# Kernel optimization log

Hardware: AMD Instinct MI355X
Metric: run time of the kernel (lower is better)

Reference implementation:

```python
import jax, jax.numpy as jnp
import numpy as np

B, L, D = 4, 512, 768
NUM_SPANS = 4096
MAX_WIDTH = 8
DFF = 4 * D


def setup_inputs() -> dict:
    key = jax.random.key(0)
    k_h, k_s, k_w, k1, k2 = jax.random.split(key, 5)
    h = jax.random.normal(k_h, (B, L, D), dtype=jnp.float32)
    starts = jax.random.randint(k_s, (B, NUM_SPANS), 0, L)
    widths = jax.random.randint(k_w, (B, NUM_SPANS), 1, MAX_WIDTH + 1)
    ends = jnp.minimum(starts + widths - 1, L - 1)
    span_idx = jnp.stack([starts, ends], axis=-1).astype(jnp.int64 if jax.config.jax_enable_x64 else jnp.int32)
    W1 = jax.random.normal(k1, (D, DFF), dtype=jnp.float32) * (1.0 / np.sqrt(D))
    b1 = jnp.zeros((DFF,), dtype=jnp.float32)
    W2 = jax.random.normal(k2, (DFF, D), dtype=jnp.float32) * (1.0 / np.sqrt(DFF))
    b2 = jnp.zeros((D,), dtype=jnp.float32)
    return {"h": h, "span_idx": span_idx, "W1": W1, "b1": b1, "W2": W2, "b2": b2,
            "max_width": MAX_WIDTH}


def reference(h, span_idx, W1, b1, W2, b2, max_width):
    # h: [B, L, D]; span_idx: [B, S, 2] (start, end inclusive)
    Bv, Lv, Dv = h.shape
    starts = span_idx[:, :, 0]                       # [B, S]
    lengths = span_idx[:, :, 1] - starts + 1         # [B, S]
    offsets = jnp.arange(max_width)                  # static bound on span length
    positions = starts[:, :, None] + offsets[None, None, :]      # [B, S, W]
    mask = offsets[None, None, :] < lengths[:, :, None]          # [B, S, W]
    positions = jnp.clip(positions * mask, 0, Lv - 1)
    # indexed gather-reduce (no [B,S,L,D] broadcast): [B, S, W, D]
    gathered = h[jnp.arange(Bv)[:, None, None], positions]
    summed = jnp.sum(gathered * mask[..., None].astype(h.dtype), axis=2)  # [B, S, D]
    span_reps = summed / lengths[..., None].astype(h.dtype)
    # projection: Linear -> ReLU -> (Dropout: identity at eval) -> Linear
    hmid = jax.nn.relu(jnp.einsum('bsd,df->bsf', span_reps, W1) + b1)
    out = jnp.einsum('bsf,fd->bsd', hmid, W2) + b2
    return out
```

## Files before the change

kernel.cpp:

```cpp
#include <hip/hip_runtime.h>
#include <stdint.h>

#define B_DIM 4
#define L_DIM 512
#define D_DIM 768
#define S_DIM 4096
#define DFF_DIM 3072
#define M_DIM (B_DIM * S_DIM)

typedef unsigned short ushort_t;
typedef __attribute__((ext_vector_type(8))) short short8;
typedef __attribute__((ext_vector_type(4))) short short4v;
typedef __attribute__((ext_vector_type(4))) float floatx4;

__device__ __forceinline__ ushort_t f2bf(float x) {
  unsigned int u = __float_as_uint(x);
  u += 0x7FFFu + ((u >> 16) & 1u);
  return (ushort_t)(u >> 16);
}

__device__ __forceinline__ void load_lds16(const ushort_t* g, ushort_t* lds) {
  __builtin_amdgcn_global_load_lds(
      (const __attribute__((address_space(1))) unsigned int*)g,
      (__attribute__((address_space(3))) unsigned int*)lds, 16, 0, 0);
}

#define PIN() __builtin_amdgcn_sched_barrier(0)
#define BAR()                                  \
  do {                                         \
    PIN();                                     \
    __builtin_amdgcn_s_barrier();              \
    PIN();                                     \
  } while (0)
#define WAIT_LGKM0()                           \
  do {                                         \
    asm volatile("s_waitcnt lgkmcnt(0)");      \
    PIN();                                     \
  } while (0)
#define WAIT_VM(n)                             \
  do {                                         \
    asm volatile("s_waitcnt vmcnt(" #n ")");   \
    PIN();                                     \
  } while (0)

__device__ __forceinline__ void transpose_body(const float* __restrict__ in,
                                               ushort_t* __restrict__ out,
                                               int K, int N, int kb, int nb) {
  __shared__ float tile[32][33];
  const int k0 = kb * 32;
  const int n0 = nb * 32;
  const int tx = threadIdx.x & 31;
  const int ty = threadIdx.x >> 5;
#pragma unroll
  for (int r = 0; r < 32; r += 8)
    tile[ty + r][tx] = in[(long)(k0 + ty + r) * N + n0 + tx];
  __syncthreads();
#pragma unroll
  for (int r = 0; r < 32; r += 8)
    out[(long)(n0 + ty + r) * K + k0 + tx] = f2bf(tile[tx][ty + r]);
}

__device__ __forceinline__ void span_body(const float* __restrict__ h,
                                          const int* __restrict__ span_idx,
                                          ushort_t* __restrict__ A, int blk) {
  const int wave = threadIdx.x >> 6;
  const int lane = threadIdx.x & 63;
  const int span = blk * 4 + wave;
  const int b = span >> 12;
  const int start = span_idx[span * 2 + 0];
  const int end   = span_idx[span * 2 + 1];
  const float inv = 1.0f / (float)(end - start + 1);
  const floatx4* hb = (const floatx4*)(h + (long)b * L_DIM * D_DIM) + lane;
  floatx4 a[3];
#pragma unroll
  for (int c = 0; c < 3; ++c) a[c] = (floatx4)0.0f;
  for (int p = start; p <= end; p += 2) {
    const int p1 = (p + 1 <= end) ? p + 1 : p;
    const float m1 = (p + 1 <= end) ? 1.0f : 0.0f;
    const floatx4* h0 = hb + (long)p * 192;
    const floatx4* h1 = hb + (long)p1 * 192;
    floatx4 v0[3], v1[3];
#pragma unroll
    for (int c = 0; c < 3; ++c) v0[c] = h0[c * 64];
#pragma unroll
    for (int c = 0; c < 3; ++c) v1[c] = h1[c * 64];
#pragma unroll
    for (int c = 0; c < 3; ++c) {
      a[c] += v0[c];
#pragma unroll
      for (int e = 0; e < 4; ++e) a[c][e] += m1 * v1[c][e];
    }
  }
  short4v* o = (short4v*)(A + (long)span * D_DIM) + lane;
#pragma unroll
  for (int c = 0; c < 3; ++c) {
    short4v s;
#pragma unroll
    for (int e = 0; e < 4; ++e) s[e] = (short)f2bf(a[c][e] * inv);
    o[c * 64] = s;
  }
}

__global__ __launch_bounds__(256)
void prep(const float* __restrict__ W1, ushort_t* __restrict__ W1T,
          const float* __restrict__ W2, ushort_t* __restrict__ W2T,
          const float* __restrict__ h, const int* __restrict__ span_idx,
          ushort_t* __restrict__ A) {
  const int blk = blockIdx.x;
  if (blk < 2304) {
    transpose_body(W1, W1T, D_DIM, DFF_DIM, blk % 24, blk / 24);
  } else if (blk < 4608) {
    const int b = blk - 2304;
    transpose_body(W2, W2T, DFF_DIM, D_DIM, b % 96, b / 96);
  } else {
    span_body(h, span_idx, A, blk - 4608);
  }
}

__global__ __launch_bounds__(512, 2)
void gemm1_p3(const ushort_t* __restrict__ A, const ushort_t* __restrict__ Bt,
              const float* __restrict__ bias, ushort_t* __restrict__ C) {
  __shared__ ushort_t As[3][128 * 64];
  __shared__ ushort_t Bs[3][256 * 64];

  const int tid  = threadIdx.x;
  const int lane = tid & 63;
  const int l16  = lane & 15;
  const int quad = lane >> 4;
  const int wave = tid >> 6;
  const int wr   = wave >> 2;
  const int wc   = wave & 3;

  const int bm = blockIdx.x;
  const int bn = blockIdx.y;

  const int srow = tid >> 3;
  const int gch  = (tid & 7) ^ (srow & 7);
  const ushort_t* gA = A  + (long)(bm * 128 + srow) * 768 + gch * 8;
  const ushort_t* gB = Bt + (long)(bn * 256 + srow) * 768 + gch * 8;
  const long r64 = (long)768 * 64;

  auto STAGE_A = [&](int buf, int kt) {
    const long ko = (long)kt * 64;
    ushort_t* la = &As[buf][0] + tid * 8;
    load_lds16(gA + ko,       la);
    load_lds16(gA + ko + r64, la + 4096);
  };
  auto STAGE_B01 = [&](int buf, int kt) {
    const long ko = (long)kt * 64;
    ushort_t* lb = &Bs[buf][0] + tid * 8;
    load_lds16(gB + ko,       lb);
    load_lds16(gB + ko + r64, lb + 4096);
  };
  auto STAGE_B23 = [&](int buf, int kt) {
    const long ko = (long)kt * 64;
    ushort_t* lb = &Bs[buf][0] + tid * 8;
    load_lds16(gB + ko + 2 * r64, lb + 8192);
    load_lds16(gB + ko + 3 * r64, lb + 12288);
  };

  const int arow0 = (wr * 64 + l16) * 64;
  const int brow0 = (wc * 64 + l16) * 64;
  const int cx0 = ((quad)     ^ (l16 & 7)) << 3;
  const int cx1 = ((quad + 4) ^ (l16 & 7)) << 3;

  floatx4 acc[4][4];
#pragma unroll
  for (int i = 0; i < 4; ++i)
#pragma unroll
    for (int j = 0; j < 4; ++j) acc[i][j] = (floatx4)0.0f;

  const int nk = 12;

  STAGE_A(0, 0); STAGE_B01(0, 0); STAGE_B23(0, 0);
  STAGE_A(1, 1); STAGE_B01(1, 1); STAGE_B23(1, 1);
  WAIT_VM(6);
  BAR();

  short8 a0[2][2], a2[2][2], b0[2][2], b2[2][2];
  int cur = 0;

  for (int k = 0; k < nk; ++k) {
    const int s2 = (cur + 2 >= 3) ? cur - 1 : cur + 2;
    const ushort_t* Ac = &As[cur][0];
    const ushort_t* Bc = &Bs[cur][0];
    const bool pf = (k + 2 < nk);

#pragma unroll
    for (int i = 0; i < 2; ++i) {
      a0[i][0] = *(const short8*)(Ac + arow0 + i * 1024 + cx0);
      a0[i][1] = *(const short8*)(Ac + arow0 + i * 1024 + cx1);
    }
#pragma unroll
    for (int j = 0; j < 2; ++j) {
      b0[j][0] = *(const short8*)(Bc + brow0 + j * 1024 + cx0);
      b0[j][1] = *(const short8*)(Bc + brow0 + j * 1024 + cx1);
    }
    if (pf) STAGE_A(s2, k + 2);
    BAR();
    WAIT_LGKM0();
    __builtin_amdgcn_s_setprio(1);
#pragma unroll
    for (int i = 0; i < 2; ++i)
#pragma unroll
      for (int j = 0; j < 2; ++j) {
        acc[i][j] = __builtin_amdgcn_mfma_f32_16x16x32_bf16(a0[i][0], b0[j][0], acc[i][j], 0, 0, 0);
        acc[i][j] = __builtin_amdgcn_mfma_f32_16x16x32_bf16(a0[i][1], b0[j][1], acc[i][j], 0, 0, 0);
      }
    __builtin_amdgcn_s_setprio(0);

#pragma unroll
    for (int j = 0; j < 2; ++j) {
      b2[j][0] = *(const short8*)(Bc + brow0 + (2 + j) * 1024 + cx0);
      b2[j][1] = *(const short8*)(Bc + brow0 + (2 + j) * 1024 + cx1);
    }
    if (pf) STAGE_B01(s2, k + 2);
    BAR();
    WAIT_LGKM0();
    __builtin_amdgcn_s_setprio(1);
#pragma unroll
    for (int i = 0; i < 2; ++i)
#pragma unroll
      for (int j = 0; j < 2; ++j) {
        acc[i][2 + j] = __builtin_amdgcn_mfma_f32_16x16x32_bf16(a0[i][0], b2[j][0], acc[i][2 + j], 0, 0, 0);
        acc[i][2 + j] = __builtin_amdgcn_mfma_f32_16x16x32_bf16(a0[i][1], b2[j][1], acc[i][2 + j], 0, 0, 0);
      }
    __builtin_amdgcn_s_setprio(0);

#pragma unroll
    for (int i = 0; i < 2; ++i) {
      a2[i][0] = *(const short8*)(Ac + arow0 + (2 + i) * 1024 + cx0);
      a2[i][1] = *(const short8*)(Ac + arow0 + (2 + i) * 1024 + cx1);
    }
    if (pf) STAGE_B23(s2, k + 2);
    BAR();
    WAIT_LGKM0();
    __builtin_amdgcn_s_setprio(1);
#pragma unroll
    for (int i = 0; i < 2; ++i)
#pragma unroll
      for (int j = 0; j < 2; ++j) {
        acc[2 + i][2 + j] = __builtin_amdgcn_mfma_f32_16x16x32_bf16(a2[i][0], b2[j][0], acc[2 + i][2 + j], 0, 0, 0);
        acc[2 + i][2 + j] = __builtin_amdgcn_mfma_f32_16x16x32_bf16(a2[i][1], b2[j][1], acc[2 + i][2 + j], 0, 0, 0);
      }
    __builtin_amdgcn_s_setprio(0);

    if (pf) {
      WAIT_VM(6);
    } else {
      WAIT_VM(0);
    }
    BAR();
    __builtin_amdgcn_s_setprio(1);
#pragma unroll
    for (int i = 0; i < 2; ++i)
#pragma unroll
      for (int j = 0; j < 2; ++j) {
        acc[2 + i][j] = __builtin_amdgcn_mfma_f32_16x16x32_bf16(a2[i][0], b0[j][0], acc[2 + i][j], 0, 0, 0);
        acc[2 + i][j] = __builtin_amdgcn_mfma_f32_16x16x32_bf16(a2[i][1], b0[j][1], acc[2 + i][j], 0, 0, 0);
      }
    __builtin_amdgcn_s_setprio(0);

    cur = (cur + 1 >= 3) ? 0 : cur + 1;
  }

  const long rowbase = (long)bm * 128 + wr * 64 + quad * 4;
  const int  colbase = bn * 256 + wc * 64 + l16;
#pragma unroll
  for (int j = 0; j < 4; ++j) {
    const int col = colbase + j * 16;
    const float bv = bias[col];
#pragma unroll
    for (int i = 0; i < 4; ++i) {
      const long row0 = rowbase + i * 16;
#pragma unroll
      for (int r = 0; r < 4; ++r) {
        float v = acc[i][j][r] + bv;
        v = v > 0.0f ? v : 0.0f;
        C[(row0 + r) * DFF_DIM + col] = f2bf(v);
      }
    }
  }
}

template <int MODE>
__global__ __launch_bounds__(256)
void gemm_bt(const ushort_t* __restrict__ A, const ushort_t* __restrict__ Bt,
             const float* __restrict__ bias, void* __restrict__ Cv,
             int M, int N, int K) {
  __shared__ ushort_t As[2][128 * 32];
  __shared__ ushort_t Bs[2][128 * 32];

  const int tid  = threadIdx.x;
  const int lane = tid & 63;
  const int wave = tid >> 6;
  const int l16  = lane & 15;
  const int quad = lane >> 4;

  const int bm = blockIdx.x;
  const int bn = blockIdx.y;

  const int wm = (wave & 1) * 64;
  const int wn = (wave >> 1) * 64;

  const int swz  = (l16 & 3) ^ ((l16 >> 2) & 3);
  const int coff = (quad ^ swz) * 8;

  floatx4 acc[4][4];
#pragma unroll
  for (int i = 0; i < 4; ++i)
#pragma unroll
    for (int j = 0; j < 4; ++j)
      acc[i][j] = (floatx4)0.0f;

  const int s0 = tid, s1 = tid + 256;
  const int r0 = s0 >> 2, r1 = s1 >> 2;
  const int c0 = (s0 & 3) ^ (r0 & 3) ^ ((r0 >> 2) & 3);
  const int c1 = (s1 & 3) ^ (r1 & 3) ^ ((r1 >> 2) & 3);
  const ushort_t* gA0 = A + (long)(bm * 128 + r0) * K + c0 * 8;
  const ushort_t* gA1 = A + (long)(bm * 128 + r1) * K + c1 * 8;
  const ushort_t* gB0 = Bt + (long)(bn * 128 + r0) * K + c0 * 8;
  const ushort_t* gB1 = Bt + (long)(bn * 128 + r1) * K + c1 * 8;

  const int nk = K >> 5;

  load_lds16(gA0, &As[0][0] + s0 * 8);
  load_lds16(gA1, &As[0][0] + s1 * 8);
  load_lds16(gB0, &Bs[0][0] + s0 * 8);
  load_lds16(gB1, &Bs[0][0] + s1 * 8);

  for (int k = 0; k < nk; ++k) {
    const int cur = k & 1;
    const int nxt = cur ^ 1;
    __syncthreads();

    if (k + 1 < nk) {
      const int off = (k + 1) * 32;
      load_lds16(gA0 + off, &As[nxt][0] + s0 * 8);
      load_lds16(gA1 + off, &As[nxt][0] + s1 * 8);
      load_lds16(gB0 + off, &Bs[nxt][0] + s0 * 8);
      load_lds16(gB1 + off, &Bs[nxt][0] + s1 * 8);
    }

    short8 af[4], bf[4];
#pragma unroll
    for (int i = 0; i < 4; ++i)
      af[i] = *(const short8*)(&As[cur][0] + (wm + i * 16 + l16) * 32 + coff);
#pragma unroll
    for (int j = 0; j < 4; ++j)
      bf[j] = *(const short8*)(&Bs[cur][0] + (wn + j * 16 + l16) * 32 + coff);
#pragma unroll
    for (int i = 0; i < 4; ++i)
#pragma unroll
      for (int j = 0; j < 4; ++j)
        acc[i][j] = __builtin_amdgcn_mfma_f32_16x16x32_bf16(af[i], bf[j], acc[i][j], 0, 0, 0);
  }

#pragma unroll
  for (int i = 0; i < 4; ++i) {
#pragma unroll
    for (int j = 0; j < 4; ++j) {
      const int col = bn * 128 + wn + j * 16 + l16;
      const float bv = bias[col];
      const int row0 = bm * 128 + wm + i * 16 + quad * 4;
#pragma unroll
      for (int r = 0; r < 4; ++r) {
        float v = acc[i][j][r] + bv;
        if (MODE == 0) {
          v = v > 0.0f ? v : 0.0f;
          ((ushort_t*)Cv)[(long)(row0 + r) * N + col] = f2bf(v);
        } else {
          ((float*)Cv)[(long)(row0 + r) * N + col] = v;
        }
      }
    }
  }
}

extern "C" void kernel_launch(void* const* d_in, const int* in_sizes, int n_in,
                              void* d_out, int out_size, void* d_ws, size_t ws_size,
                              hipStream_t stream) {
  const float* h        = (const float*)d_in[0];
  const int*   span_idx = (const int*)d_in[1];
  const float* W1       = (const float*)d_in[2];
  const float* b1       = (const float*)d_in[3];
  const float* W2       = (const float*)d_in[4];
  const float* b2       = (const float*)d_in[5];
  float* out = (float*)d_out;

  ushort_t* A   = (ushort_t*)d_ws;
  ushort_t* W1T = A + (size_t)M_DIM * D_DIM;
  ushort_t* W2T = W1T + (size_t)DFF_DIM * D_DIM;
  ushort_t* Hm  = W2T + (size_t)D_DIM * DFF_DIM;

  prep<<<2304 + 2304 + M_DIM / 4, 256, 0, stream>>>(W1, W1T, W2, W2T, h, span_idx, A);

  gemm1_p3<<<dim3(M_DIM / 128, DFF_DIM / 256), 512, 0, stream>>>(A, W1T, b1, Hm);

  gemm_bt<1><<<dim3(M_DIM / 128, D_DIM / 128), 256, 0, stream>>>(
      Hm, W2T, b2, out, M_DIM, D_DIM, DFF_DIM);
}
```

Baseline: 276.4 us.

## Move W2 transpose into gemm1 grid as tail blocks to overlap with GEMM

The W2 fp32-to-bf16 transpose moves out of the prep kernel and into extra blocks appended to the gemm1 launch, which now uses a 1D grid with manual bm/bn decoding. The intent is to shorten the serialized prep phase and let the transpose fill idle CUs during the tail of gemm1. The epilogue loop order is also reordered so bias values are loaded once into registers. The transpose blocks reuse gemm1's large LDS allocation and 512-thread shape, which may cost occupancy for that part of the work.

```diff
diff --git a/kernel.cpp b/kernel.cpp
--- a/kernel.cpp
+++ b/kernel.cpp
@@ -103,27 +103,48 @@
 
 __global__ __launch_bounds__(256)
 void prep(const float* __restrict__ W1, ushort_t* __restrict__ W1T,
-          const float* __restrict__ W2, ushort_t* __restrict__ W2T,
           const float* __restrict__ h, const int* __restrict__ span_idx,
           ushort_t* __restrict__ A) {
   const int blk = blockIdx.x;
   if (blk < 2304) {
     transpose_body(W1, W1T, D_DIM, DFF_DIM, blk % 24, blk / 24);
-  } else if (blk < 4608) {
-    const int b = blk - 2304;
-    transpose_body(W2, W2T, DFF_DIM, D_DIM, b % 96, b / 96);
   } else {
-    span_body(h, span_idx, A, blk - 4608);
+    span_body(h, span_idx, A, blk - 2304);
   }
 }
 
 __global__ __launch_bounds__(512, 2)
 void gemm1_p3(const ushort_t* __restrict__ A, const ushort_t* __restrict__ Bt,
-              const float* __restrict__ bias, ushort_t* __restrict__ C) {
+              const float* __restrict__ bias, ushort_t* __restrict__ C,
+              const float* __restrict__ W2, ushort_t* __restrict__ W2T) {
   __shared__ ushort_t As[3][128 * 64];
   __shared__ ushort_t Bs[3][256 * 64];
 
-  const int tid  = threadIdx.x;
+  const int tid = threadIdx.x;
+  const int blk = blockIdx.x;
+
+  if (blk >= 1536) {
+    const int half = tid >> 8;
+    const int ttid = tid & 255;
+    const int tx = ttid & 31, ty = ttid >> 5;
+    float* scratch = (float*)&As[0][0] + half * (32 * 33);
+#pragma unroll
+    for (int it = 0; it < 4; ++it) {
+      const int tile = (blk - 1536) * 8 + half * 4 + it;
+      const int kb = tile % 96, nb = tile / 96;
+      const int k0 = kb * 32, n0 = nb * 32;
+#pragma unroll
+      for (int r = 0; r < 32; r += 8)
+        scratch[(ty + r) * 33 + tx] = W2[(long)(k0 + ty + r) * 768 + n0 + tx];
+      __syncthreads();
+#pragma unroll
+      for (int r = 0; r < 32; r += 8)
+        W2T[(long)(n0 + ty + r) * 3072 + k0 + tx] = f2bf(scratch[tx * 33 + ty + r]);
+      __syncthreads();
+    }
+    return;
+  }
+
   const int lane = tid & 63;
   const int l16  = lane & 15;
   const int quad = lane >> 4;
@@ -131,8 +152,8 @@
   const int wr   = wave >> 2;
   const int wc   = wave & 3;
 
-  const int bm = blockIdx.x;
-  const int bn = blockIdx.y;
+  const int bm = blk & 127;
+  const int bn = blk >> 7;
 
   const int srow = tid >> 3;
   const int gch  = (tid & 7) ^ (srow & 7);
@@ -266,18 +287,19 @@
 
   const long rowbase = (long)bm * 128 + wr * 64 + quad * 4;
   const int  colbase = bn * 256 + wc * 64 + l16;
-#pragma unroll
-  for (int j = 0; j < 4; ++j) {
-    const int col = colbase + j * 16;
-    const float bv = bias[col];
-#pragma unroll
-    for (int i = 0; i < 4; ++i) {
-      const long row0 = rowbase + i * 16;
-#pragma unroll
-      for (int r = 0; r < 4; ++r) {
-        float v = acc[i][j][r] + bv;
+  float bv[4];
+#pragma unroll
+  for (int j = 0; j < 4; ++j) bv[j] = bias[colbase + j * 16];
+#pragma unroll
+  for (int i = 0; i < 4; ++i) {
+#pragma unroll
+    for (int r = 0; r < 4; ++r) {
+      const long row = rowbase + i * 16 + r;
+#pragma unroll
+      for (int j = 0; j < 4; ++j) {
+        float v = acc[i][j][r] + bv[j];
         v = v > 0.0f ? v : 0.0f;
-        C[(row0 + r) * DFF_DIM + col] = f2bf(v);
+        C[row * DFF_DIM + colbase + j * 16] = f2bf(v);
       }
     }
   }
@@ -393,9 +415,9 @@
   ushort_t* W2T = W1T + (size_t)DFF_DIM * D_DIM;
   ushort_t* Hm  = W2T + (size_t)D_DIM * DFF_DIM;
 
-  prep<<<2304 + 2304 + M_DIM / 4, 256, 0, stream>>>(W1, W1T, W2, W2T, h, span_idx, A);
-
-  gemm1_p3<<<dim3(M_DIM / 128, DFF_DIM / 256), 512, 0, stream>>>(A, W1T, b1, Hm);
+  prep<<<2304 + M_DIM / 4, 256, 0, stream>>>(W1, W1T, h, span_idx, A);
+
+  gemm1_p3<<<1536 + 288, 512, 0, stream>>>(A, W1T, b1, Hm, W2, W2T);
 
   gemm_bt<1><<<dim3(M_DIM / 128, D_DIM / 128), 256, 0, stream>>>(
       Hm, W2T, b2, out, M_DIM, D_DIM, DFF_DIM);
```

Result: no change. 278.0 us (+0.6%).
